# Kernel optimization log

Measured on AMD Instinct MI355X. Metric: run time of the kernel, lower is better.

Reference implementation:

```python
import jax, jax.numpy as jnp
import numpy as np

MEMORY_SIZE = 2000
SHAPE = (512, 8, 8)
D = int(np.prod(SHAPE))  # 32768
LAM = 0.0005  # hard-shrink threshold (1/memory_size convention)
EPS = 1e-12   # F.normalize eps


def _l2_normalize(x, axis):
    # matches F.normalize(p=2): x / max(||x||, eps)
    n = jnp.sqrt(jnp.sum(x * x, axis=axis, keepdims=True))
    return x / jnp.maximum(n, EPS)


def _hard_shrink(x):
    return jnp.where(jnp.abs(x) > LAM, x, jnp.zeros_like(x))


def setup_inputs() -> dict:
    key = jax.random.key(0)
    k1, k2 = jax.random.split(key)
    feature = jax.random.normal(k1, (256, *SHAPE), dtype=jnp.float32)
    memory = jax.random.normal(k2, (MEMORY_SIZE, D), dtype=jnp.float32)
    return {"feature": feature, "memory": memory}


def reference(feature, memory):
    B = feature.shape[0]
    flat = feature.reshape(B, -1)                     # [B, D]
    fn = _l2_normalize(flat, axis=1)                  # [B, D]
    mn = _l2_normalize(memory, axis=1)                # [M, D]
    w = jnp.einsum('bd,md->bm', fn, mn)               # cosine similarity [B, M]
    w = jax.nn.softmax(w, axis=1)
    w = _hard_shrink(w)
    w = jax.nn.softmax(w, axis=1)
    mem_feat = jnp.einsum('bm,md->bd', w, memory)     # [B, D]
    mem_feat = mem_feat.reshape(B, *SHAPE)
    return (mem_feat, w)
```

## Files before the change

kernel.cpp:

```cpp
#include <hip/hip_runtime.h>
#include <math.h>


#define D_DIM 32768
#define B_DIM 256
#define M_DIM 2000
#define M_PAD 2048
#define NS1 16
#define KSLAB (D_DIM / NS1)
#define LAM 0.0005f
#define LDB 72

typedef __attribute__((ext_vector_type(8))) short bf16x8;
typedef __attribute__((ext_vector_type(4))) float f32x4;

#define GLOBAL_AS __attribute__((address_space(1)))
#define LDS_AS __attribute__((address_space(3)))

__device__ __forceinline__ void cp_async16(const void* g, void* l) {
  __builtin_amdgcn_global_load_lds((const GLOBAL_AS unsigned int*)g,
                                   (LDS_AS unsigned int*)l, 16, 0, 0);
}

__device__ __forceinline__ unsigned short f2bf(float f) {
  union { float f; unsigned u; } v; v.f = f;
  unsigned r = v.u + 0x7FFFu + ((v.u >> 16) & 1u);
  return (unsigned short)(r >> 16);
}

__global__ __launch_bounds__(256) void zero_kernel(float* __restrict__ p, int n) {
  int i = blockIdx.x * 256 + threadIdx.x;
  if (i < n) p[i] = 0.f;
}

__global__ __launch_bounds__(256) void prep_feat_kernel(const float* __restrict__ src,
                                                        unsigned short* __restrict__ dst,
                                                        float* __restrict__ rn_inv) {
  const size_t row = blockIdx.x;
  const int t = threadIdx.x;
  const float4* p = (const float4*)(src + row * (size_t)D_DIM);
  ushort4* q = (ushort4*)(dst + row * (size_t)D_DIM);
  float s = 0.f;
  for (int i = t; i < D_DIM / 4; i += 256) {
    float4 v = p[i];
    s = fmaf(v.x, v.x, s); s = fmaf(v.y, v.y, s);
    s = fmaf(v.z, v.z, s); s = fmaf(v.w, v.w, s);
    ushort4 b; b.x = f2bf(v.x); b.y = f2bf(v.y); b.z = f2bf(v.z); b.w = f2bf(v.w);
    q[i] = b;
  }
  #pragma unroll
  for (int off = 32; off > 0; off >>= 1) s += __shfl_down(s, off, 64);
  __shared__ float partial[4];
  if ((t & 63) == 0) partial[t >> 6] = s;
  __syncthreads();
  if (t == 0) {
    float tt = partial[0] + partial[1] + partial[2] + partial[3];
    rn_inv[row] = 1.0f / fmaxf(sqrtf(tt), 1e-12f);
  }
}

__global__ __launch_bounds__(256, 3) void gemm1_fused(const unsigned short* __restrict__ F16,
                                                      const float* __restrict__ mem,
                                                      float* __restrict__ Spart,
                                                      float* __restrict__ rnm_sq) {
  __shared__ __align__(16) unsigned short Asm[256 * 64];
  __shared__ __align__(16) unsigned short Bsm[64 * LDB];
  const int t = threadIdx.x;
  const int m0 = blockIdx.x * 64;
  const int kbase = blockIdx.y * KSLAB;
  const int wid = t >> 6, lane = t & 63;
  const int lr = lane & 15, kq = lane >> 4;
  const int l8 = lane & 7, lrow = lane >> 3;

  const int brow = t >> 2;
  const int bcol = (t & 3) * 16;
  const int gm = m0 + brow;
  const bool bvalid = gm < M_DIM;
  const float* Bg = mem + (size_t)gm * D_DIM + kbase + bcol;

  const unsigned short* Ab = F16 + (size_t)(64 * wid + lrow) * D_DIM + kbase + (l8 ^ lrow) * 8;

  f32x4 acc[4][4] = {};
  float ss = 0.f;

  for (int kt = 0; kt < KSLAB / 64; kt++) {
    const int kk = kt * 64;
    __syncthreads();
    #pragma unroll
    for (int i = 0; i < 8; i++)
      cp_async16(Ab + kk + (size_t)(8 * i) * D_DIM, &Asm[(64 * wid + 8 * i) * 64]);

    float4 v[4];
    #pragma unroll
    for (int j = 0; j < 4; j++)
      v[j] = bvalid ? *(const float4*)(Bg + kk + 4 * j) : make_float4(0.f, 0.f, 0.f, 0.f);
    #pragma unroll
    for (int j = 0; j < 4; j++) {
      ss = fmaf(v[j].x, v[j].x, ss); ss = fmaf(v[j].y, v[j].y, ss);
      ss = fmaf(v[j].z, v[j].z, ss); ss = fmaf(v[j].w, v[j].w, ss);
      ushort4 c; c.x = f2bf(v[j].x); c.y = f2bf(v[j].y);
      c.z = f2bf(v[j].z); c.w = f2bf(v[j].w);
      *(ushort4*)&Bsm[brow * LDB + bcol + 4 * j] = c;
    }
    __syncthreads();

    bf16x8 bfr[2][4];
    #pragma unroll
    for (int h = 0; h < 2; h++)
      #pragma unroll
      for (int ni = 0; ni < 4; ni++)
        bfr[h][ni] = *(const bf16x8*)&Bsm[(ni * 16 + lr) * LDB + h * 32 + kq * 8];
    #pragma unroll
    for (int mi = 0; mi < 4; mi++) {
      #pragma unroll
      for (int h = 0; h < 2; h++) {
        const int sw = ((h * 4 + kq) ^ (lr & 7)) * 8;
        const bf16x8 af = *(const bf16x8*)&Asm[(wid * 64 + mi * 16 + lr) * 64 + sw];
        #pragma unroll
        for (int ni = 0; ni < 4; ni++)
          acc[mi][ni] = __builtin_amdgcn_mfma_f32_16x16x32_bf16(af, bfr[h][ni], acc[mi][ni], 0, 0, 0);
      }
    }
  }

  ss += __shfl_down(ss, 2, 4);
  ss += __shfl_down(ss, 1, 4);
  if ((t & 3) == 0 && bvalid) atomicAdd(&rnm_sq[gm], ss);

  float* Sp = Spart + (size_t)blockIdx.y * (B_DIM * M_PAD);
  #pragma unroll
  for (int mi = 0; mi < 4; mi++) {
    const int b0 = wid * 64 + mi * 16 + kq * 4;
    #pragma unroll
    for (int ni = 0; ni < 4; ni++) {
      const int col = m0 + ni * 16 + lr;
      #pragma unroll
      for (int j = 0; j < 4; j++)
        Sp[(size_t)(b0 + j) * M_PAD + col] = acc[mi][ni][j];
    }
  }
}

__device__ __forceinline__ float block_reduce(float x, bool is_max, float* red,
                                              int wid, int lane) {
  #pragma unroll
  for (int off = 32; off > 0; off >>= 1) {
    float o = __shfl_down(x, off, 64);
    x = is_max ? fmaxf(x, o) : (x + o);
  }
  __syncthreads();
  if (lane == 0) red[wid] = x;
  __syncthreads();
  return is_max ? fmaxf(fmaxf(red[0], red[1]), fmaxf(red[2], red[3]))
                : (red[0] + red[1] + red[2] + red[3]);
}

__global__ __launch_bounds__(256) void softmax_kernel(const float* __restrict__ Spart,
                                                      const float* __restrict__ rnf,
                                                      const float* __restrict__ rnm_sq,
                                                      float* __restrict__ wout,
                                                      unsigned short* __restrict__ wbf) {
  const int b = blockIdx.x;
  const int t = threadIdx.x;
  const int wid = t >> 6, lane = t & 63;
  const float sf = rnf[b];
  __shared__ float red[4];

  float v[8];
  #pragma unroll
  for (int g = 0; g < 2; g++) {
    const int mq = g * 1024 + 4 * t;
    f32x4 a = {0.f, 0.f, 0.f, 0.f};
    #pragma unroll
    for (int s = 0; s < NS1; s++)
      a += *(const f32x4*)&Spart[(size_t)s * (B_DIM * M_PAD) + (size_t)b * M_PAD + mq];
    #pragma unroll
    for (int j = 0; j < 4; j++) {
      const int m = mq + j;
      const float msc = 1.0f / fmaxf(sqrtf(rnm_sq[m]), 1e-12f);
      v[g * 4 + j] = (m < M_DIM) ? a[j] * (sf * msc) : -INFINITY;
    }
  }
  float mx = v[0];
  #pragma unroll
  for (int i = 1; i < 8; i++) mx = fmaxf(mx, v[i]);
  mx = block_reduce(mx, true, red, wid, lane);

  float e[8]; float sum = 0.f;
  #pragma unroll
  for (int i = 0; i < 8; i++) { e[i] = expf(v[i] - mx); sum += e[i]; }
  sum = block_reduce(sum, false, red, wid, lane);
  const float inv = 1.f / sum;

  float s2[8];
  #pragma unroll
  for (int i = 0; i < 8; i++) {
    float w1 = e[i] * inv;
    s2[i] = (w1 > LAM) ? w1 : 0.f;
  }
  float mx2 = 0.f;
  #pragma unroll
  for (int i = 0; i < 8; i++) mx2 = fmaxf(mx2, s2[i]);
  mx2 = block_reduce(mx2, true, red, wid, lane);

  float e2[8]; float sum2 = 0.f;
  #pragma unroll
  for (int g = 0; g < 2; g++)
    #pragma unroll
    for (int j = 0; j < 4; j++) {
      const int i = g * 4 + j;
      const int m = g * 1024 + 4 * t + j;
      e2[i] = (m < M_DIM) ? expf(s2[i] - mx2) : 0.f;
      sum2 += e2[i];
    }
  sum2 = block_reduce(sum2, false, red, wid, lane);
  const float inv2 = 1.f / sum2;

  #pragma unroll
  for (int g = 0; g < 2; g++) {
    const int mq = g * 1024 + 4 * t;
    float4 wq; ushort4 bq;
    float* wp = (float*)&wq;
    #pragma unroll
    for (int j = 0; j < 4; j++) {
      const float w2 = e2[g * 4 + j] * inv2;
      wp[j] = w2;
      ((unsigned short*)&bq)[j] = f2bf(w2);
    }
    if (mq + 3 < M_DIM) *(float4*)&wout[(size_t)b * M_DIM + mq] = wq;
    *(ushort4*)&wbf[(size_t)b * M_PAD + mq] = bq;
  }
}

__global__ __launch_bounds__(256, 3) void gemm2_kernel(const unsigned short* __restrict__ W,
                                                       const float* __restrict__ mem,
                                                       float* __restrict__ C) {
  __shared__ __align__(16) unsigned short Wsm[256 * 64];
  __shared__ __align__(16) unsigned short Bt[64 * 64];
  const int t = threadIdx.x;
  const int n0 = blockIdx.x * 64;
  const int wid = t >> 6, lane = t & 63;
  const int lr = lane & 15, kq = lane >> 4;
  const int l8 = lane & 7, lrow = lane >> 3;

  const unsigned short* Wb = W + (size_t)(64 * wid + lrow) * M_PAD + (l8 ^ lrow) * 8;

  const int bn = t & 63;
  const int kc = t >> 6;
  const float* Bg = mem + (size_t)(kc * 16) * D_DIM + n0 + bn;

  f32x4 acc[4][4] = {};

  for (int k0 = 0; k0 < M_PAD; k0 += 64) {
    __syncthreads();
    #pragma unroll
    for (int i = 0; i < 8; i++)
      cp_async16(Wb + k0 + (size_t)(8 * i) * M_PAD, &Wsm[(64 * wid + 8 * i) * 64]);

    bf16x8 kb0, kb1;
    #pragma unroll
    for (int j = 0; j < 8; j++) {
      const int k = k0 + kc * 16 + j;
      const float f = (k < M_DIM) ? Bg[(size_t)(k0 + j) * D_DIM] : 0.f;
      kb0[j] = (short)f2bf(f);
    }
    #pragma unroll
    for (int j = 8; j < 16; j++) {
      const int k = k0 + kc * 16 + j;
      const float f = (k < M_DIM) ? Bg[(size_t)(k0 + j) * D_DIM] : 0.f;
      kb1[j - 8] = (short)f2bf(f);
    }
    *(bf16x8*)&Bt[bn * 64 + (((kc * 2 + 0) ^ (bn & 7)) * 8)] = kb0;
    *(bf16x8*)&Bt[bn * 64 + (((kc * 2 + 1) ^ (bn & 7)) * 8)] = kb1;
    __syncthreads();

    bf16x8 bfr[2][4];
    #pragma unroll
    for (int h = 0; h < 2; h++)
      #pragma unroll
      for (int ni = 0; ni < 4; ni++)
        bfr[h][ni] = *(const bf16x8*)&Bt[(ni * 16 + lr) * 64 + (((h * 4 + kq) ^ (lr & 7)) * 8)];
    #pragma unroll
    for (int mi = 0; mi < 4; mi++) {
      #pragma unroll
      for (int h = 0; h < 2; h++) {
        const int sw = ((h * 4 + kq) ^ (lr & 7)) * 8;
        const bf16x8 af = *(const bf16x8*)&Wsm[(wid * 64 + mi * 16 + lr) * 64 + sw];
        #pragma unroll
        for (int ni = 0; ni < 4; ni++)
          acc[mi][ni] = __builtin_amdgcn_mfma_f32_16x16x32_bf16(af, bfr[h][ni], acc[mi][ni], 0, 0, 0);
      }
    }
  }
  #pragma unroll
  for (int mi = 0; mi < 4; mi++) {
    const int b0 = wid * 64 + mi * 16 + kq * 4;
    #pragma unroll
    for (int ni = 0; ni < 4; ni++) {
      const int col = n0 + ni * 16 + lr;
      #pragma unroll
      for (int j = 0; j < 4; j++)
        C[(size_t)(b0 + j) * D_DIM + col] = acc[mi][ni][j];
    }
  }
}

extern "C" void kernel_launch(void* const* d_in, const int* in_sizes, int n_in,
                              void* d_out, int out_size, void* d_ws, size_t ws_size,
                              hipStream_t stream) {
  const float* feature = (const float*)d_in[0];
  const float* memory  = (const float*)d_in[1];
  float* out_feat = (float*)d_out;
  float* out_w = out_feat + (size_t)B_DIM * D_DIM;

  char* ws = (char*)d_ws;
  unsigned short* F16 = (unsigned short*)ws;
  float* Spart        = (float*)(ws + 16777216ull);
  unsigned short* Wbf = (unsigned short*)(ws + 50331648ull);
  float* rnm_sq       = (float*)(ws + 51380224ull);
  float* rnf          = (float*)(ws + 51388416ull);

  zero_kernel<<<(M_PAD + 255) / 256, 256, 0, stream>>>(rnm_sq, M_PAD);
  prep_feat_kernel<<<B_DIM, 256, 0, stream>>>(feature, F16, rnf);
  gemm1_fused<<<dim3(M_PAD / 64, NS1), 256, 0, stream>>>(F16, memory, Spart, rnm_sq);
  softmax_kernel<<<B_DIM, 256, 0, stream>>>(Spart, rnf, rnm_sq, out_w, Wbf);
  gemm2_kernel<<<D_DIM / 64, 256, 0, stream>>>(Wbf, memory, out_feat);
}
```

Before: 491.2 us.

## Double-buffer LDS and register-prefetch next tiles in both GEMM kernels

Both GEMM kernels gain a second LDS buffer for the A/W tile. The next k-tile's async global-to-LDS copy and its fp32 B loads are issued before the MFMAs on the current tile, so memory latency overlaps compute instead of sitting behind a barrier each iteration. Out-of-range rows are clamped to row 0 rather than zeroed. For the padded M rows in gemm2 this relies on the padded W entries being zero. The doubled shared memory and extra prefetch registers lower the launch-bounds occupancy hint from 3 to 2 blocks per CU, which trades latency hiding by occupancy for explicit prefetch.

```diff
diff --git a/kernel.cpp b/kernel.cpp
--- a/kernel.cpp
+++ b/kernel.cpp
@@ -59,11 +59,11 @@
   }
 }
 
-__global__ __launch_bounds__(256, 3) void gemm1_fused(const unsigned short* __restrict__ F16,
+__global__ __launch_bounds__(256, 2) void gemm1_fused(const unsigned short* __restrict__ F16,
                                                       const float* __restrict__ mem,
                                                       float* __restrict__ Spart,
                                                       float* __restrict__ rnm_sq) {
-  __shared__ __align__(16) unsigned short Asm[256 * 64];
+  __shared__ __align__(16) unsigned short Asm[2][256 * 64];
   __shared__ __align__(16) unsigned short Bsm[64 * LDB];
   const int t = threadIdx.x;
   const int m0 = blockIdx.x * 64;
@@ -76,24 +76,23 @@
   const int bcol = (t & 3) * 16;
   const int gm = m0 + brow;
   const bool bvalid = gm < M_DIM;
-  const float* Bg = mem + (size_t)gm * D_DIM + kbase + bcol;
+  const float* Bg = mem + (size_t)(bvalid ? gm : 0) * D_DIM + kbase + bcol;
 
   const unsigned short* Ab = F16 + (size_t)(64 * wid + lrow) * D_DIM + kbase + (l8 ^ lrow) * 8;
 
   f32x4 acc[4][4] = {};
   float ss = 0.f;
 
-  for (int kt = 0; kt < KSLAB / 64; kt++) {
-    const int kk = kt * 64;
-    __syncthreads();
-    #pragma unroll
-    for (int i = 0; i < 8; i++)
-      cp_async16(Ab + kk + (size_t)(8 * i) * D_DIM, &Asm[(64 * wid + 8 * i) * 64]);
-
-    float4 v[4];
-    #pragma unroll
-    for (int j = 0; j < 4; j++)
-      v[j] = bvalid ? *(const float4*)(Bg + kk + 4 * j) : make_float4(0.f, 0.f, 0.f, 0.f);
+  #pragma unroll
+  for (int i = 0; i < 8; i++)
+    cp_async16(Ab + (size_t)(8 * i) * D_DIM, &Asm[0][(64 * wid + 8 * i) * 64]);
+  float4 v[4];
+  #pragma unroll
+  for (int j = 0; j < 4; j++) v[j] = *(const float4*)(Bg + 4 * j);
+
+  int cur = 0;
+  const int NT = KSLAB / 64;
+  for (int kt = 0; kt < NT; kt++) {
     #pragma unroll
     for (int j = 0; j < 4; j++) {
       ss = fmaf(v[j].x, v[j].x, ss); ss = fmaf(v[j].y, v[j].y, ss);
@@ -104,6 +103,16 @@
     }
     __syncthreads();
 
+    float4 vn[4];
+    if (kt + 1 < NT) {
+      const int kk = (kt + 1) * 64;
+      #pragma unroll
+      for (int i = 0; i < 8; i++)
+        cp_async16(Ab + kk + (size_t)(8 * i) * D_DIM, &Asm[cur ^ 1][(64 * wid + 8 * i) * 64]);
+      #pragma unroll
+      for (int j = 0; j < 4; j++) vn[j] = *(const float4*)(Bg + kk + 4 * j);
+    }
+
     bf16x8 bfr[2][4];
     #pragma unroll
     for (int h = 0; h < 2; h++)
@@ -115,12 +124,18 @@
       #pragma unroll
       for (int h = 0; h < 2; h++) {
         const int sw = ((h * 4 + kq) ^ (lr & 7)) * 8;
-        const bf16x8 af = *(const bf16x8*)&Asm[(wid * 64 + mi * 16 + lr) * 64 + sw];
+        const bf16x8 af = *(const bf16x8*)&Asm[cur][(wid * 64 + mi * 16 + lr) * 64 + sw];
         #pragma unroll
         for (int ni = 0; ni < 4; ni++)
           acc[mi][ni] = __builtin_amdgcn_mfma_f32_16x16x32_bf16(af, bfr[h][ni], acc[mi][ni], 0, 0, 0);
       }
     }
+    __syncthreads();
+    if (kt + 1 < NT) {
+      #pragma unroll
+      for (int j = 0; j < 4; j++) v[j] = vn[j];
+    }
+    cur ^= 1;
   }
 
   ss += __shfl_down(ss, 2, 4);
@@ -232,10 +247,10 @@
   }
 }
 
-__global__ __launch_bounds__(256, 3) void gemm2_kernel(const unsigned short* __restrict__ W,
+__global__ __launch_bounds__(256, 2) void gemm2_kernel(const unsigned short* __restrict__ W,
                                                        const float* __restrict__ mem,
                                                        float* __restrict__ C) {
-  __shared__ __align__(16) unsigned short Wsm[256 * 64];
+  __shared__ __align__(16) unsigned short Wsm[2][256 * 64];
   __shared__ __align__(16) unsigned short Bt[64 * 64];
   const int t = threadIdx.x;
   const int n0 = blockIdx.x * 64;
@@ -247,33 +262,46 @@
 
   const int bn = t & 63;
   const int kc = t >> 6;
-  const float* Bg = mem + (size_t)(kc * 16) * D_DIM + n0 + bn;
+  const float* Bg2 = mem + n0 + bn;
 
   f32x4 acc[4][4] = {};
 
-  for (int k0 = 0; k0 < M_PAD; k0 += 64) {
-    __syncthreads();
-    #pragma unroll
-    for (int i = 0; i < 8; i++)
-      cp_async16(Wb + k0 + (size_t)(8 * i) * M_PAD, &Wsm[(64 * wid + 8 * i) * 64]);
-
+  #pragma unroll
+  for (int i = 0; i < 8; i++)
+    cp_async16(Wb + (size_t)(8 * i) * M_PAD, &Wsm[0][(64 * wid + 8 * i) * 64]);
+  float bv[16];
+  #pragma unroll
+  for (int j = 0; j < 16; j++) {
+    const int k = kc * 16 + j;
+    bv[j] = Bg2[(size_t)k * D_DIM];
+  }
+
+  int cur = 0;
+  const int NT = M_PAD / 64;
+  for (int it = 0; it < NT; it++) {
     bf16x8 kb0, kb1;
     #pragma unroll
-    for (int j = 0; j < 8; j++) {
-      const int k = k0 + kc * 16 + j;
-      const float f = (k < M_DIM) ? Bg[(size_t)(k0 + j) * D_DIM] : 0.f;
-      kb0[j] = (short)f2bf(f);
-    }
-    #pragma unroll
-    for (int j = 8; j < 16; j++) {
-      const int k = k0 + kc * 16 + j;
-      const float f = (k < M_DIM) ? Bg[(size_t)(k0 + j) * D_DIM] : 0.f;
-      kb1[j - 8] = (short)f2bf(f);
-    }
+    for (int j = 0; j < 8; j++) kb0[j] = (short)f2bf(bv[j]);
+    #pragma unroll
+    for (int j = 0; j < 8; j++) kb1[j] = (short)f2bf(bv[8 + j]);
     *(bf16x8*)&Bt[bn * 64 + (((kc * 2 + 0) ^ (bn & 7)) * 8)] = kb0;
     *(bf16x8*)&Bt[bn * 64 + (((kc * 2 + 1) ^ (bn & 7)) * 8)] = kb1;
     __syncthreads();
 
+    float bvn[16];
+    if (it + 1 < NT) {
+      const int kn = it * 64 + 64;
+      #pragma unroll
+      for (int i = 0; i < 8; i++)
+        cp_async16(Wb + kn + (size_t)(8 * i) * M_PAD, &Wsm[cur ^ 1][(64 * wid + 8 * i) * 64]);
+      #pragma unroll
+      for (int j = 0; j < 16; j++) {
+        const int k = kn + kc * 16 + j;
+        const int r = (k < M_DIM) ? k : 0;
+        bvn[j] = Bg2[(size_t)r * D_DIM];
+      }
+    }
+
     bf16x8 bfr[2][4];
     #pragma unroll
     for (int h = 0; h < 2; h++)
@@ -285,12 +313,18 @@
       #pragma unroll
       for (int h = 0; h < 2; h++) {
         const int sw = ((h * 4 + kq) ^ (lr & 7)) * 8;
-        const bf16x8 af = *(const bf16x8*)&Wsm[(wid * 64 + mi * 16 + lr) * 64 + sw];
+        const bf16x8 af = *(const bf16x8*)&Wsm[cur][(wid * 64 + mi * 16 + lr) * 64 + sw];
         #pragma unroll
         for (int ni = 0; ni < 4; ni++)
           acc[mi][ni] = __builtin_amdgcn_mfma_f32_16x16x32_bf16(af, bfr[h][ni], acc[mi][ni], 0, 0, 0);
       }
     }
+    __syncthreads();
+    if (it + 1 < NT) {
+      #pragma unroll
+      for (int j = 0; j < 16; j++) bv[j] = bvn[j];
+    }
+    cur ^= 1;
   }
   #pragma unroll
   for (int mi = 0; mi < 4; mi++) {
```

New measurement: 492.5 us. Within noise of the previous version (+0.3%).
